# Kernel optimization log

Hardware: AMD Instinct MI355X
Metric: run time of the kernel (lower is better)

The kernel has to match this reference:

```python
import jax, jax.numpy as jnp
import numpy as np

S, B, I, H, O = 512, 64, 256, 1024, 128

def setup_inputs() -> dict:
    key = jax.random.key(0)
    ks = jax.random.split(key, 9)
    std0 = 1.0 / np.sqrt(H)
    inp = {
        "x": jax.random.normal(ks[0], (S, B, I), dtype=jnp.float32),
        "W_r0": jax.random.normal(ks[1], (H, I + H), dtype=jnp.float32) * std0,
        "b_r0": jnp.zeros((H,), jnp.float32),
        "W_z0": jax.random.normal(ks[2], (H, I + H), dtype=jnp.float32) * std0,
        "b_z0": jnp.zeros((H,), jnp.float32),
        "W_h0": jax.random.normal(ks[3], (H, I + H), dtype=jnp.float32) * std0,
        "b_h0": jnp.zeros((H,), jnp.float32),
        "W_r1": jax.random.normal(ks[4], (H, H + H), dtype=jnp.float32) * std0,
        "b_r1": jnp.zeros((H,), jnp.float32),
        "W_z1": jax.random.normal(ks[5], (H, H + H), dtype=jnp.float32) * std0,
        "b_z1": jnp.zeros((H,), jnp.float32),
        "W_h1": jax.random.normal(ks[6], (H, H + H), dtype=jnp.float32) * std0,
        "b_h1": jnp.zeros((H,), jnp.float32),
        "W_out": jax.random.normal(ks[7], (O, H), dtype=jnp.float32) * (1.0 / np.sqrt(H)),
        "b_out": jax.random.normal(ks[8], (O,), dtype=jnp.float32) * (1.0 / np.sqrt(H)),
    }
    return inp

def _gru_cell(x, h, W_r, b_r, W_z, b_z, W_h, b_h):
    # x: [B, in], h: [B, H]
    comb = jnp.concatenate([x, h], axis=1)
    r = jax.nn.sigmoid(comb @ W_r.T + b_r)
    z = jax.nn.sigmoid(comb @ W_z.T + b_z)
    rc = jnp.concatenate([x, r * h], axis=1)
    h_tilde = jnp.tanh(rc @ W_h.T + b_h)
    return (1.0 - z) * h + z * h_tilde

def reference(x, W_r0, b_r0, W_z0, b_z0, W_h0, b_h0,
              W_r1, b_r1, W_z1, b_z1, W_h1, b_h1, W_out, b_out):
    batch = x.shape[1]
    h0_init = jnp.zeros((batch, H), x.dtype)
    h1_init = jnp.zeros((batch, H), x.dtype)

    def step(carry, x_t):
        h0, h1 = carry
        h0 = _gru_cell(x_t, h0, W_r0, b_r0, W_z0, b_z0, W_h0, b_h0)
        h1 = _gru_cell(h0, h1, W_r1, b_r1, W_z1, b_z1, W_h1, b_h1)
        out_t = h1 @ W_out.T + b_out  # [B, O]
        return (h0, h1), out_t

    (h0_f, h1_f), outputs = jax.lax.scan(step, (h0_init, h1_init), x)
    return outputs, jnp.stack([h0_f, h1_f], axis=0)  # [S,B,O], [L,B,H]
```

## Files before the change

### kernel.cpp

```cpp
#include <hip/hip_runtime.h>

#define SLEN 512
#define BATCH 64
#define IDIM 256
#define HDIM 1024
#define ODIM 128
#define NBLK 256
#define NTHR 512
#define AGENT __HIP_MEMORY_SCOPE_AGENT
#define SLOTB 1605632ull

typedef unsigned short ushortT;
typedef unsigned long long ull;
typedef __attribute__((ext_vector_type(8))) short short8;
typedef __attribute__((ext_vector_type(4))) float f32x4;

__device__ __forceinline__ ushortT f2bf(float f) {
  unsigned u = __float_as_uint(f);
  unsigned r = (u + 0x7FFFu + ((u >> 16) & 1u)) >> 16;
  return (ushortT)r;
}

__device__ __forceinline__ void pack2(const float* __restrict__ s, ushortT* d) {
  float4 a = *(const float4*)s;
  float4 b = *(const float4*)(s + 16);
  short8 v;
  v[0]=(short)f2bf(a.x); v[1]=(short)f2bf(a.y); v[2]=(short)f2bf(a.z); v[3]=(short)f2bf(a.w);
  v[4]=(short)f2bf(b.x); v[5]=(short)f2bf(b.y); v[6]=(short)f2bf(b.z); v[7]=(short)f2bf(b.w);
  *(short8*)d = v;
}

__device__ __forceinline__ void pack2a(const float* __restrict__ s, ushortT* d) {
  float4 a = *(const float4*)s;
  float4 b = *(const float4*)(s + 16);
  ull lo = (ull)f2bf(a.x) | ((ull)f2bf(a.y) << 16) | ((ull)f2bf(a.z) << 32) | ((ull)f2bf(a.w) << 48);
  ull hi = (ull)f2bf(b.x) | ((ull)f2bf(b.y) << 16) | ((ull)f2bf(b.z) << 32) | ((ull)f2bf(b.w) << 48);
  __hip_atomic_store((ull*)d, lo, __ATOMIC_RELAXED, AGENT);
  __hip_atomic_store((ull*)(d + 4), hi, __ATOMIC_RELAXED, AGENT);
}

__device__ __forceinline__ void mir_store(ushortT* M, int row, int cL, float v) {
  int kt = cL >> 5, c5 = cL & 31;
  int h = c5 >> 4, g = (c5 >> 2) & 3, j = c5 & 3;
  int u = ((kt * 4 + (row >> 4)) * 64) + 16 * g + (row & 15);
  __hip_atomic_store(&M[(size_t)u * 8 + h * 4 + j], f2bf(v), __ATOMIC_RELAXED, AGENT);
}

__device__ __forceinline__ void st_f32x4(float* p, float v0, float v1, float v2, float v3) {
  ull lo = (ull)__float_as_uint(v0) | ((ull)__float_as_uint(v1) << 32);
  ull hi = (ull)__float_as_uint(v2) | ((ull)__float_as_uint(v3) << 32);
  __hip_atomic_store((ull*)p, lo, __ATOMIC_RELAXED, AGENT);
  __hip_atomic_store((ull*)(p + 2), hi, __ATOMIC_RELAXED, AGENT);
}

__device__ __forceinline__ void gsync(unsigned* sy, int blk, int tid, unsigned idx, bool acq) {
  __syncthreads();
  if (tid == 0)
    __hip_atomic_store(&sy[16 * blk], idx, __ATOMIC_RELAXED, AGENT);
  if (tid < 256) {
    while (__hip_atomic_load(&sy[16 * tid], __ATOMIC_RELAXED, AGENT) < idx)
      __builtin_amdgcn_s_sleep(1);
  }
  __syncthreads();
  if (acq) {
    if (tid == 0) __hip_atomic_load(&sy[16 * blk], __ATOMIC_ACQUIRE, AGENT);
    __syncthreads();
  }
}

__device__ __forceinline__ float fold8(float v) {
  v += __shfl_xor(v, 8);
  v += __shfl_xor(v, 16);
  v += __shfl_xor(v, 32);
  return v;
}

template<int NKT, int SPLIT, int NC>
__device__ __forceinline__ f32x4 stage_mm16(
    const ushortT* __restrict__ mA, const ushortT* __restrict__ mB,
    const ushortT* WL, float (*red)[64][4], int l, int w)
{
  const int mt = w & 3, kh = w >> 2;
  constexpr int H = NKT / 2;
  const int lo = kh * H;
  const int g = l >> 4, col = l & 15;
  f32x4 acc = {0.f, 0.f, 0.f, 0.f};
  short8 af[H];
  #pragma unroll
  for (int t = 0; t < H; ++t) {
    const int kt = lo + t;
    const ushortT* p = (kt < SPLIT)
        ? mA + (size_t)((kt * 4 + mt) * 64 + l) * 8
        : mB + (size_t)(((kt - SPLIT) * 4 + mt) * 64 + l) * 8;
    af[t] = *(const short8*)p;
  }
  #pragma unroll
  for (int t = 0; t < H; ++t) {
    short8 b = {0,0,0,0,0,0,0,0};
    if (col < NC)
      b = *(const short8*)(&WL[(size_t)(((lo + t) * 4 + g) * NC + col) * 8]);
    acc = __builtin_amdgcn_mfma_f32_16x16x32_bf16(af[t], b, acc, 0, 0, 0);
  }
  if (w >= 4) *(f32x4*)&red[w - 4][l][0] = acc;
  __syncthreads();
  if (w < 4) { f32x4 o = *(f32x4*)&red[w][l][0]; acc += o; }
  return acc;
}

__device__ __forceinline__ void out_dot(const ushortT* __restrict__ Mh1p,
                                        const ushortT* WLo, float bo,
                                        float* __restrict__ out,
                                        int s_store, int jo, int tid) {
  const int l = tid & 63, w = tid >> 6;
  const int rr = (w << 3) + (l & 7);
  const int ks = l >> 3;
  const int mt = rr >> 4, r15 = rr & 15;
  float a0 = 0.f;
  #pragma unroll
  for (int q = 0; q < 4; ++q) {
    const int kt = (ks << 2) + q;
    #pragma unroll
    for (int gg = 0; gg < 4; ++gg) {
      const int u = ((kt << 2) + mt) * 64 + (gg << 4) + r15;
      union { short8 v; ushortT us[8]; } M;
      M.v = *(const short8*)(Mh1p + (size_t)u * 8);
      ull wlo = *(const ull*)(WLo + kt * 36 + (gg << 2));
      ull whi = *(const ull*)(WLo + kt * 36 + 16 + (gg << 2));
      #pragma unroll
      for (int j = 0; j < 4; ++j) {
        float mv = __uint_as_float(((unsigned)M.us[j]) << 16);
        float wv = __uint_as_float((unsigned)((wlo >> (16 * j)) & 0xFFFFu) << 16);
        a0 = fmaf(mv, wv, a0);
      }
      #pragma unroll
      for (int j = 0; j < 4; ++j) {
        float mv = __uint_as_float(((unsigned)M.us[4 + j]) << 16);
        float wv = __uint_as_float((unsigned)((whi >> (16 * j)) & 0xFFFFu) << 16);
        a0 = fmaf(mv, wv, a0);
      }
    }
  }
  float v = fold8(a0);
  if ((l & 56) == 0)
    out[((size_t)s_store * BATCH + rr) * ODIM + jo] = v + bo;
}

__global__ __launch_bounds__(NTHR, 2) void gru_pipe(
    const float* __restrict__ x,
    const float* __restrict__ Wr0, const float* __restrict__ br0,
    const float* __restrict__ Wz0, const float* __restrict__ bz0,
    const float* __restrict__ Wh0, const float* __restrict__ bh0,
    const float* __restrict__ Wr1, const float* __restrict__ br1,
    const float* __restrict__ Wz1, const float* __restrict__ bz1,
    const float* __restrict__ Wh1, const float* __restrict__ bh1,
    const float* __restrict__ Wout, const float* __restrict__ bout,
    float* __restrict__ out, char* __restrict__ ws, int nrot)
{
  __shared__ ushortT WSH[53248];
  __shared__ float red[4][64][4];

  const int blk = blockIdx.x;
  const int tid = threadIdx.x;
  const int l = tid & 63;
  const int w = tid >> 6;
  const int g = l >> 4;
  const int colL = l & 15;
  const int rowb = (w << 4) + (g << 2);

  unsigned* sy = (unsigned*)ws;
  char* slots = ws + 16384;

  ushortT* WA = WSH;
  ushortT* WB = WSH + (blk < 128 ? 20480 : 32768);

  if (blk < 128) {
    const int j0 = blk * 8;
    for (int u = tid; u < 40 * 4 * 16; u += NTHR) {
      int kt = u >> 6, gg = (u >> 4) & 3, c = u & 15;
      const float* src = (c < 8 ? Wr0 + (size_t)(j0 + c) * 1280
                                : Wz0 + (size_t)(j0 + c - 8) * 1280) + kt * 32 + gg * 4;
      pack2(src, &WA[(size_t)u * 8]);
    }
  } else {
    const int j1 = (blk - 128) * 8;
    for (int u = tid; u < 64 * 4 * 16; u += NTHR) {
      int kt = u >> 6, gg = (u >> 4) & 3, c = u & 15;
      const float* src = (c < 8 ? Wr1 + (size_t)(j1 + c) * 2048
                                : Wz1 + (size_t)(j1 + c - 8) * 2048) + kt * 32 + gg * 4;
      pack2(src, &WA[(size_t)u * 8]);
    }
  }
  if (blk < 64) {
    const int c0 = blk * 16;
    for (int u = tid; u < 40 * 4 * 16; u += NTHR) {
      int kt = u >> 6, gg = (u >> 4) & 3, c = u & 15;
      pack2(Wh0 + (size_t)(c0 + c) * 1280 + kt * 32 + gg * 4, &WB[(size_t)u * 8]);
    }
  } else if (blk < 128) {
    const int c0 = (blk - 64) * 16;
    for (int u = tid; u < 64 * 4 * 16; u += NTHR) {
      int kt = u >> 6, gg = (u >> 4) & 3, c = u & 15;
      pack2(Wh1 + (size_t)(c0 + c) * 2048 + kt * 32 + gg * 4, &WB[(size_t)u * 8]);
    }
  } else {
    for (int u = tid; u < 256; u += NTHR) {
      float4 a = *(const float4*)(Wout + (size_t)(blk - 128) * HDIM + (u << 2));
      int kt = u >> 3, c4 = (u & 7) << 2;
      ushortT* dst = &WB[kt * 36 + c4];
      dst[0] = f2bf(a.x); dst[1] = f2bf(a.y); dst[2] = f2bf(a.z); dst[3] = f2bf(a.w);
    }
  }
  if (blk >= 128 && tid < 16) {
    ushortT* Mx0 = (ushortT*)(slots + 1572864);
    int u = ((blk - 128) << 4) + tid;
    int kt = u >> 8, mtu = (u >> 6) & 3, lane = u & 63;
    int row = (mtu << 4) + (lane & 15), gg = lane >> 4;
    pack2a(x + (size_t)row * IDIM + (kt << 5) + (gg << 2), Mx0 + (size_t)u * 8);
  }

  float biasA = 0.f, biasB = 0.f, bo = 0.f;
  int cgA = 0, cgB = 0;
  if (blk < 128) {
    cgA = (blk << 3) + (colL & 7);
    biasA = (colL < 8) ? br0[cgA] : bz0[cgA];
  } else {
    cgA = ((blk - 128) << 3) + (colL & 7);
    biasA = (colL < 8) ? br1[cgA] : bz1[cgA];
  }
  if (blk < 64)       { cgB = (blk << 4) + colL;        biasB = bh0[cgB]; }
  else if (blk < 128) { cgB = ((blk - 64) << 4) + colL; biasB = bh1[cgB]; }
  else                { bo = bout[blk - 128]; }

  unsigned sidx = 0;
  gsync(sy, blk, tid, ++sidx, true);

  for (int i = 0; i <= SLEN; ++i) {
    const int pc = i % nrot;
    const int pp = (i + nrot - 1) % nrot;
    const int pn = (i + 1) % nrot;
    char* Spc = slots + SLOTB * pc;
    char* Spp = slots + SLOTB * pp;

    const float* h0prev = (const float*)Spp;
    float*       h0cur  = (float*)Spc;
    const float* h1prev = (const float*)(Spp + 262144);
    float*       h1cur  = (float*)(Spc + 262144);
    float* z0f = (float*)(Spc + 524288);
    float* z1f = (float*)(Spc + 786432);
    const ushortT* Mh0p = (const ushortT*)(Spp + 1048576);
    ushortT*       Mh0w = (ushortT*)(Spc + 1048576);
    const ushortT* Mh1p = (const ushortT*)(Spp + 1179648);
    ushortT*       Mh1w = (ushortT*)(Spc + 1179648);
    ushortT* Mrh0 = (ushortT*)(Spc + 1310720);
    ushortT* Mrh1 = (ushortT*)(Spc + 1441792);
    const ushortT* MxP = (const ushortT*)(Spc + 1572864);
    ushortT*       MxW = (ushortT*)(slots + SLOTB * pn + 1572864);

    if (blk < 128) {
      if (i < SLEN) {
        float4 hq = {0.f, 0.f, 0.f, 0.f};
        if (w < 4 && colL < 8)
          hq = *(const float4*)(h0prev + (size_t)cgA * 64 + rowb);
        f32x4 acc = stage_mm16<40, 8, 16>(MxP, Mh0p, WA, red, l, w);
        if (w < 4) {
          float sg[4];
          #pragma unroll
          for (int r = 0; r < 4; ++r)
            sg[r] = 1.f / (1.f + __expf(-(acc[r] + biasA)));
          if (colL < 8) {
            mir_store(Mrh0, rowb + 0, cgA, sg[0] * hq.x);
            mir_store(Mrh0, rowb + 1, cgA, sg[1] * hq.y);
            mir_store(Mrh0, rowb + 2, cgA, sg[2] * hq.z);
            mir_store(Mrh0, rowb + 3, cgA, sg[3] * hq.w);
          } else {
            st_f32x4(z0f + (size_t)cgA * 64 + rowb, sg[0], sg[1], sg[2], sg[3]);
          }
        }
      }
    } else {
      if (i >= 1) {
        float4 hq = {0.f, 0.f, 0.f, 0.f};
        if (w < 4 && colL < 8)
          hq = *(const float4*)(h1prev + (size_t)cgA * 64 + rowb);
        f32x4 acc = stage_mm16<64, 32, 16>(Mh0p, Mh1p, WA, red, l, w);
        if (w < 4) {
          float sg[4];
          #pragma unroll
          for (int r = 0; r < 4; ++r)
            sg[r] = 1.f / (1.f + __expf(-(acc[r] + biasA)));
          if (colL < 8) {
            mir_store(Mrh1, rowb + 0, cgA, sg[0] * hq.x);
            mir_store(Mrh1, rowb + 1, cgA, sg[1] * hq.y);
            mir_store(Mrh1, rowb + 2, cgA, sg[2] * hq.z);
            mir_store(Mrh1, rowb + 3, cgA, sg[3] * hq.w);
          } else {
            st_f32x4(z1f + (size_t)cgA * 64 + rowb, sg[0], sg[1], sg[2], sg[3]);
          }
        }
      }
    }
    gsync(sy, blk, tid, ++sidx, (i % nrot) == 0);

    if (blk < 64) {
      if (i < SLEN) {
        float4 zq = {0.f, 0.f, 0.f, 0.f}, hq = {0.f, 0.f, 0.f, 0.f};
        if (w < 4) {
          zq = *(const float4*)(z0f + (size_t)cgB * 64 + rowb);
          hq = *(const float4*)(h0prev + (size_t)cgB * 64 + rowb);
        }
        f32x4 acc = stage_mm16<40, 8, 16>(MxP, Mrh0, WB, red, l, w);
        if (w < 4) {
          float hn[4];
          const float hpv[4] = {hq.x, hq.y, hq.z, hq.w};
          const float zv[4] = {zq.x, zq.y, zq.z, zq.w};
          #pragma unroll
          for (int r = 0; r < 4; ++r) {
            float ht = tanhf(acc[r] + biasB);
            hn[r] = fmaf(zv[r], ht - hpv[r], hpv[r]);
            mir_store(Mh0w, rowb + r, cgB, hn[r]);
          }
          st_f32x4(h0cur + (size_t)cgB * 64 + rowb, hn[0], hn[1], hn[2], hn[3]);
        }
      }
    } else if (blk < 128) {
      if (i >= 1) {
        float4 zq = {0.f, 0.f, 0.f, 0.f}, hq = {0.f, 0.f, 0.f, 0.f};
        if (w < 4) {
          zq = *(const float4*)(z1f + (size_t)cgB * 64 + rowb);
          hq = *(const float4*)(h1prev + (size_t)cgB * 64 + rowb);
        }
        f32x4 acc = stage_mm16<64, 32, 16>(Mh0p, Mrh1, WB, red, l, w);
        if (w < 4) {
          float hn[4];
          const float hpv[4] = {hq.x, hq.y, hq.z, hq.w};
          const float zv[4] = {zq.x, zq.y, zq.z, zq.w};
          #pragma unroll
          for (int r = 0; r < 4; ++r) {
            float ht = tanhf(acc[r] + biasB);
            hn[r] = fmaf(zv[r], ht - hpv[r], hpv[r]);
            mir_store(Mh1w, rowb + r, cgB, hn[r]);
          }
          st_f32x4(h1cur + (size_t)cgB * 64 + rowb, hn[0], hn[1], hn[2], hn[3]);
        }
      }
    } else {
      if (i + 1 < SLEN && tid < 16) {
        int u = ((blk - 128) << 4) + tid;
        int kt = u >> 8, mtu = (u >> 6) & 3, lane = u & 63;
        int row = (mtu << 4) + (lane & 15), gg = lane >> 4;
        pack2a(x + ((size_t)(i + 1) * BATCH + row) * IDIM + (kt << 5) + (gg << 2),
               MxW + (size_t)u * 8);
      }
      if (i >= 2)
        out_dot(Mh1p, WB, bo, out, i - 2, blk - 128, tid);
    }
    gsync(sy, blk, tid, ++sidx, ((i + 1) % nrot) == 0 || i == SLEN);
  }

  {
    char* Sf1 = slots + SLOTB * (SLEN % nrot);
    char* Sf0 = slots + SLOTB * ((SLEN - 1) % nrot);
    if (blk >= 128)
      out_dot((const ushortT*)(Sf1 + 1179648), WB, bo, out, SLEN - 1, blk - 128, tid);
    const float* h0fin = (const float*)Sf0;
    const float* h1fin = (const float*)(Sf1 + 262144);
    const size_t base = (size_t)SLEN * BATCH * ODIM;
    const int u = blk * NTHR + tid;
    float v;
    if (u < 65536) {
      int row = u >> 10, col = u & 1023;
      v = h0fin[(size_t)col * 64 + row];
    } else {
      int t = u - 65536;
      int row = t >> 10, col = t & 1023;
      v = h1fin[(size_t)col * 64 + row];
    }
    out[base + u] = v;
  }
}

extern "C" void kernel_launch(void* const* d_in, const int* in_sizes, int n_in,
                              void* d_out, int out_size, void* d_ws, size_t ws_size,
                              hipStream_t stream) {
  const float* xx  = (const float*)d_in[0];
  const float* Wr0 = (const float*)d_in[1];
  const float* br0 = (const float*)d_in[2];
  const float* Wz0 = (const float*)d_in[3];
  const float* bz0 = (const float*)d_in[4];
  const float* Wh0 = (const float*)d_in[5];
  const float* bh0 = (const float*)d_in[6];
  const float* Wr1 = (const float*)d_in[7];
  const float* br1 = (const float*)d_in[8];
  const float* Wz1 = (const float*)d_in[9];
  const float* bz1 = (const float*)d_in[10];
  const float* Wh1 = (const float*)d_in[11];
  const float* bh1 = (const float*)d_in[12];
  const float* Wou = (const float*)d_in[13];
  const float* bou = (const float*)d_in[14];

  long long avail = (long long)ws_size - 16384;
  int nrot = (int)(avail / (long long)SLOTB);
  if (nrot > 16) nrot = 16;
  if (nrot < 2) nrot = 2;

  hipMemsetAsync(d_ws, 0, 16384 + (size_t)nrot * SLOTB, stream);

  gru_pipe<<<dim3(NBLK), dim3(NTHR), 0, stream>>>(
      xx, Wr0, br0, Wz0, bz0, Wh0, bh0,
      Wr1, br1, Wz1, bz1, Wh1, bh1, Wou, bou,
      (float*)d_out, (char*)d_ws, nrot);
}
```

Baseline: 6.970 ms.

## Replace all-block grid barriers with targeted dependency waits

Each full grid barrier becomes an arrive plus a wait on only the producer blocks whose data the next phase reads. Gate blocks for layer 0 wait on blocks 0-127 and those for layer 1 on blocks 128-255, while output blocks skip the mid-step wait. The x-packing work moves ahead of the layer-1 gate computation. The aim is to cut barrier latency and let the independent block groups run ahead of one another. Correctness now depends on the dependency sets being complete, including slot reuse across the rotation, and a final full wait is added before the epilogue.

```diff
diff --git a/kernel.cpp b/kernel.cpp
--- a/kernel.cpp
+++ b/kernel.cpp
@@ -53,26 +53,27 @@
   __hip_atomic_store((ull*)(p + 2), hi, __ATOMIC_RELAXED, AGENT);
 }
 
-__device__ __forceinline__ void gsync(unsigned* sy, int blk, int tid, unsigned idx, bool acq) {
+__device__ __forceinline__ void arrive(unsigned* sy, int blk, int tid, unsigned idx) {
   __syncthreads();
   if (tid == 0)
     __hip_atomic_store(&sy[16 * blk], idx, __ATOMIC_RELAXED, AGENT);
-  if (tid < 256) {
-    while (__hip_atomic_load(&sy[16 * tid], __ATOMIC_RELAXED, AGENT) < idx)
+}
+
+__device__ __forceinline__ void wait2(unsigned* sy, int tid,
+                                      int b0, int n0, unsigned t0,
+                                      int b1, int n1, unsigned t1,
+                                      bool acq, int blk) {
+  int s = -1; unsigned tg = 0;
+  if (tid < n0) { s = b0 + tid; tg = t0; }
+  else if (tid < n0 + n1) { s = b1 + (tid - n0); tg = t1; }
+  if (s >= 0)
+    while (__hip_atomic_load(&sy[16 * s], __ATOMIC_RELAXED, AGENT) < tg)
       __builtin_amdgcn_s_sleep(1);
-  }
   __syncthreads();
   if (acq) {
     if (tid == 0) __hip_atomic_load(&sy[16 * blk], __ATOMIC_ACQUIRE, AGENT);
     __syncthreads();
   }
-}
-
-__device__ __forceinline__ float fold8(float v) {
-  v += __shfl_xor(v, 8);
-  v += __shfl_xor(v, 16);
-  v += __shfl_xor(v, 32);
-  return v;
 }
 
 template<int NKT, int SPLIT, int NC>
@@ -105,6 +106,13 @@
   __syncthreads();
   if (w < 4) { f32x4 o = *(f32x4*)&red[w][l][0]; acc += o; }
   return acc;
+}
+
+__device__ __forceinline__ float fold8(float v) {
+  v += __shfl_xor(v, 8);
+  v += __shfl_xor(v, 16);
+  v += __shfl_xor(v, 32);
+  return v;
 }
 
 __device__ __forceinline__ void out_dot(const ushortT* __restrict__ Mh1p,
@@ -231,8 +239,8 @@
   else if (blk < 128) { cgB = ((blk - 64) << 4) + colL; biasB = bh1[cgB]; }
   else                { bo = bout[blk - 128]; }
 
-  unsigned sidx = 0;
-  gsync(sy, blk, tid, ++sidx, true);
+  arrive(sy, blk, tid, 1u);
+  wait2(sy, tid, 0, 256, 1u, 0, 0, 0u, true, blk);
 
   for (int i = 0; i <= SLEN; ++i) {
     const int pc = i % nrot;
@@ -256,6 +264,11 @@
     const ushortT* MxP = (const ushortT*)(Spc + 1572864);
     ushortT*       MxW = (ushortT*)(slots + SLOTB * pn + 1572864);
 
+    const unsigned eA = 2u * (unsigned)i + 2u;
+    const unsigned eB = 2u * (unsigned)i + 3u;
+    const bool acqA = (i % nrot) == 0;
+    const bool acqB = ((i + 1) % nrot) == 0 || i == SLEN;
+
     if (blk < 128) {
       if (i < SLEN) {
         float4 hq = {0.f, 0.f, 0.f, 0.f};
@@ -278,6 +291,13 @@
         }
       }
     } else {
+      if (i + 1 < SLEN && tid < 16) {
+        int u = ((blk - 128) << 4) + tid;
+        int kt = u >> 8, mtu = (u >> 6) & 3, lane = u & 63;
+        int row = (mtu << 4) + (lane & 15), gg = lane >> 4;
+        pack2a(x + ((size_t)(i + 1) * BATCH + row) * IDIM + (kt << 5) + (gg << 2),
+               MxW + (size_t)u * 8);
+      }
       if (i >= 1) {
         float4 hq = {0.f, 0.f, 0.f, 0.f};
         if (w < 4 && colL < 8)
@@ -299,7 +319,10 @@
         }
       }
     }
-    gsync(sy, blk, tid, ++sidx, (i % nrot) == 0);
+    arrive(sy, blk, tid, eA);
+    if (blk < 64)        wait2(sy, tid, 0, 128, eA, 0, 0, 0u, acqA, blk);
+    else if (blk < 128)  wait2(sy, tid, 128, 128, eA, 0, 0, 0u, acqA, blk);
+    else                 wait2(sy, tid, 0, 0, 0u, 0, 0, 0u, acqA, blk);
 
     if (blk < 64) {
       if (i < SLEN) {
@@ -344,19 +367,15 @@
         }
       }
     } else {
-      if (i + 1 < SLEN && tid < 16) {
-        int u = ((blk - 128) << 4) + tid;
-        int kt = u >> 8, mtu = (u >> 6) & 3, lane = u & 63;
-        int row = (mtu << 4) + (lane & 15), gg = lane >> 4;
-        pack2a(x + ((size_t)(i + 1) * BATCH + row) * IDIM + (kt << 5) + (gg << 2),
-               MxW + (size_t)u * 8);
-      }
       if (i >= 2)
         out_dot(Mh1p, WB, bo, out, i - 2, blk - 128, tid);
     }
-    gsync(sy, blk, tid, ++sidx, ((i + 1) % nrot) == 0 || i == SLEN);
-  }
-
+    arrive(sy, blk, tid, eB);
+    if (blk < 128) wait2(sy, tid, 0, 64, eB, 128, 128, eA, acqB, blk);
+    else           wait2(sy, tid, 0, 128, eB, 0, 0, 0u, acqB, blk);
+  }
+
+  wait2(sy, tid, 0, 256, 2u * (unsigned)SLEN + 3u, 0, 0, 0u, true, blk);
   {
     char* Sf1 = slots + SLOTB * (SLEN % nrot);
     char* Sf0 = slots + SLOTB * ((SLEN - 1) % nrot);
```

Result: faster. 6.631 ms, median of 2 (-4.9%).
